# Optimization experiments

Measured on AMD Instinct MI355X. Metric: run time of the kernel, lower is better.

## Reference

```python
import jax, jax.numpy as jnp
import numpy as np

N_GRAPHS = 16
NPG = 420               # nodes per graph (fc1 expects 420*64 flatten)
N = N_GRAPHS * NPG      # 6720
DEG = 8
E = N * DEG             # 53760
HEADS = 4
IN_DIM = 2048
C1 = 1024               # per-head channels, layer 1
C2 = 64                 # layer 2 channels
OUT_DIM = 18
SLOPE = 0.2             # GATConv leaky_relu negative_slope


def _seg_softmax(scores, idx, n):
    # numerically-stable softmax over edges grouped by destination node
    m = jax.lax.stop_gradient(jax.ops.segment_max(scores, idx, num_segments=n))
    ex = jnp.exp(scores - m[idx])
    den = jax.ops.segment_sum(ex, idx, num_segments=n)
    return ex / (den[idx] + 1e-16)


def _transformer_conv(x, src, dst, wq, bq, wk, bk, wv, bv, ws, bs, heads, ch):
    # PyG TransformerConv defaults: concat=True, beta=False, root_weight=True, dropout=0
    n = x.shape[0]
    q = (x @ wq + bq).reshape(n, heads, ch)
    k = (x @ wk + bk).reshape(n, heads, ch)
    v = (x @ wv + bv).reshape(n, heads, ch)
    alpha = jnp.einsum('ehc,ehc->eh', q[dst], k[src]) / (ch ** 0.5)  # [E,H]
    alpha = _seg_softmax(alpha, dst, n)
    out = jax.ops.segment_sum(v[src] * alpha[..., None], dst, num_segments=n)  # [N,H,C]
    return out.reshape(n, heads * ch) + (x @ ws + bs)  # skip connection (lin_skip)


def _gat_conv(x, src, dst, w, a_src, a_dst, bias, heads, ch, concat):
    # PyG GATConv defaults: add_self_loops=True, negative_slope=0.2, lin has no bias
    n = x.shape[0]
    loop = jnp.arange(n, dtype=src.dtype)
    s = jnp.concatenate([src, loop])
    d = jnp.concatenate([dst, loop])
    h = (x @ w).reshape(n, heads, ch)
    es = jnp.einsum('nhc,hc->nh', h, a_src)
    ed = jnp.einsum('nhc,hc->nh', h, a_dst)
    e = jax.nn.leaky_relu(es[s] + ed[d], SLOPE)  # [E+N, H]
    alpha = _seg_softmax(e, d, n)
    out = jax.ops.segment_sum(h[s] * alpha[..., None], d, num_segments=n)  # [N,H,C]
    out = out.reshape(n, heads * ch) if concat else out.mean(axis=1)
    return out + bias


def setup_inputs() -> dict:
    key = jax.random.key(0)
    it = iter(jax.random.split(key, 64))
    def nrm(shape, scale):
        return jax.random.normal(next(it), shape, jnp.float32) * scale
    def lin(fi, fo):
        return nrm((fi, fo), float(1.0 / np.sqrt(fi)))
    p = {}
    p['x'] = nrm((N, IN_DIM), 1.0)
    p['edge_index'] = jax.random.randint(next(it), (2, E), 0, N, dtype=jnp.int32)
    for nm in ['t1_wq', 't1_wk', 't1_wv', 't1_ws']:
        p[nm] = lin(IN_DIM, HEADS * C1)
    for nm in ['t1_bq', 't1_bk', 't1_bv', 't1_bs']:
        p[nm] = jnp.zeros((HEADS * C1,), jnp.float32)
    # TransformerConv 2: 4096 -> 64, 1 head
    for nm in ['t2_wq', 't2_wk', 't2_wv', 't2_ws']:
        p[nm] = lin(HEADS * C1, C2)
    for nm in ['t2_bq', 't2_bk', 't2_bv', 't2_bs']:
        p[nm] = jnp.zeros((C2,), jnp.float32)
    p['g1_w'] = lin(IN_DIM, HEADS * C1)
    p['g1_as'] = nrm((HEADS, C1), 0.02)
    p['g1_ad'] = nrm((HEADS, C1), 0.02)
    p['g1_b'] = jnp.zeros((HEADS * C1,), jnp.float32)
    # GATConv 2: 4096 -> 64, 1 head, concat=False (mean)
    p['g2_w'] = lin(HEADS * C1, C2)
    p['g2_as'] = nrm((1, C2), 0.02)
    p['g2_ad'] = nrm((1, C2), 0.02)
    p['g2_b'] = jnp.zeros((C2,), jnp.float32)
    # MLP head
    p['fc1_w'] = lin(NPG * C2, 256); p['fc1_b'] = jnp.zeros((256,), jnp.float32)
    p['fc2_w'] = lin(256, 128);      p['fc2_b'] = jnp.zeros((128,), jnp.float32)
    p['fc3_w'] = lin(128, 64);       p['fc3_b'] = jnp.zeros((64,), jnp.float32)
    p['fc4_w'] = lin(64, OUT_DIM);   p['fc4_b'] = jnp.zeros((OUT_DIM,), jnp.float32)
    return p


def _forward(edge_index, x,
             t1_wq, t1_bq, t1_wk, t1_bk, t1_wv, t1_bv, t1_ws, t1_bs,
             t2_wq, t2_bq, t2_wk, t2_bk, t2_wv, t2_bv, t2_ws, t2_bs,
             g1_w, g1_as, g1_ad, g1_b, g2_w, g2_as, g2_ad, g2_b,
             fc1_w, fc1_b, fc2_w, fc2_b, fc3_w, fc3_b, fc4_w, fc4_b):
    src, dst = edge_index[0], edge_index[1]
    h = jax.nn.relu(_transformer_conv(x, src, dst, t1_wq, t1_bq, t1_wk, t1_bk,
                                      t1_wv, t1_bv, t1_ws, t1_bs, HEADS, C1))
    h = jax.nn.relu(_transformer_conv(h, src, dst, t2_wq, t2_bq, t2_wk, t2_bk,
                                      t2_wv, t2_bv, t2_ws, t2_bs, 1, C2))
    z = jax.nn.relu(_gat_conv(x, src, dst, g1_w, g1_as, g1_ad, g1_b, HEADS, C1, True))
    z = jax.nn.relu(_gat_conv(z, src, dst, g2_w, g2_as, g2_ad, g2_b, 1, C2, False))
    s = (h + z).reshape(-1, NPG * C2)          # [n_graphs, 26880]
    s = jax.nn.relu(s @ fc1_w + fc1_b)          # dropout = identity at eval
    s = jax.nn.relu(s @ fc2_w + fc2_b)
    s = jax.nn.relu(s @ fc3_w + fc3_b)
    return s @ fc4_w + fc4_b                    # [n_graphs, OUT_DIM]


def reference(x, edge_index,
              t1_wq, t1_bq, t1_wk, t1_bk, t1_wv, t1_bv, t1_ws, t1_bs,
              t2_wq, t2_bq, t2_wk, t2_bk, t2_wv, t2_bv, t2_ws, t2_bs,
              g1_w, g1_as, g1_ad, g1_b, g2_w, g2_as, g2_ad, g2_b,
              fc1_w, fc1_b, fc2_w, fc2_b, fc3_w, fc3_b, fc4_w, fc4_b):
    return _forward(edge_index, x,
                    t1_wq, t1_bq, t1_wk, t1_bk, t1_wv, t1_bv, t1_ws, t1_bs,
                    t2_wq, t2_bq, t2_wk, t2_bk, t2_wv, t2_bv, t2_ws, t2_bs,
                    g1_w, g1_as, g1_ad, g1_b, g2_w, g2_as, g2_ad, g2_b,
                    fc1_w, fc1_b, fc2_w, fc2_b, fc3_w, fc3_b, fc4_w, fc4_b)
```

## Files before the change

kernel.cpp:

```cpp
#include <hip/hip_runtime.h>
#include <stdint.h>
#include <stdio.h>

#define NNODES 6720
#define NEDGES 53760
#define NGRAPH 16
#define INDIM  2048
#define HEADS1 4
#define C1DIM  1024
#define D1     4096
#define C2DIM  64
#define N2     320
#define OUTDIM 18
#define SMCAP  256

typedef unsigned short u16;
typedef unsigned int   u32;

__device__ __forceinline__ float b2f(u16 u) {
  union { float f; u32 u; } v; v.u = ((u32)u) << 16; return v.f;
}
__device__ __forceinline__ u16 f2b(float f) {
  union { float f; u32 u; } v; v.f = f;
  u32 r = v.u + 0x7FFFu + ((v.u >> 16) & 1u);
  return (u16)(r >> 16);
}
__device__ __forceinline__ float ldf(const void* p, long i, int isf) {
  return isf ? ((const float*)p)[i] : b2f(((const u16*)p)[i]);
}

typedef __attribute__((ext_vector_type(8))) short bf16x8;
typedef __attribute__((ext_vector_type(4))) float f32x4;

__device__ __forceinline__ void gld_lds16(const u16* g, u16* l) {
  __builtin_amdgcn_global_load_lds((const __attribute__((address_space(1))) void*)g,
                                   (__attribute__((address_space(3))) void*)l, 16, 0, 0);
}

__global__ void detect_dtype(const u16* __restrict__ x, int* flag) {
  __shared__ int cnt;
  if (threadIdx.x == 0) cnt = 0;
  __syncthreads();
  int c = 0;
  for (int i = threadIdx.x; i < 4096; i += 256) {
    u16 u = x[2 * i];
    int e = (u >> 7) & 0xFF;
    if (e >= 118 && e <= 135) c++;
  }
  atomicAdd(&cnt, c);
  __syncthreads();
  if (threadIdx.x == 0) *flag = (cnt > 2048) ? 0 : 1;
}

__global__ void conv_any(const void* __restrict__ src, u16* __restrict__ dst,
                         long n, const int* __restrict__ flag) {
  long i = (long)blockIdx.x * 256 + threadIdx.x;
  long stride = (long)gridDim.x * 256;
  int isf = *flag;
  if (isf) {
    const float* s = (const float*)src;
    for (long j = i; j < n; j += stride) dst[j] = f2b(s[j]);
  } else {
    const u16* s = (const u16*)src;
    for (long j = i; j < n; j += stride) dst[j] = s[j];
  }
}

#define NSMALL 13
struct SmallConv {
  const void* src[NSMALL];
  u16*        dst[NSMALL];
  int         n[NSMALL];
};
__global__ void conv_small(SmallConv sc, const int* __restrict__ flag) {
  int b = blockIdx.x;
  int isf = *flag;
  const void* s = sc.src[b];
  u16* d = sc.dst[b];
  int n = sc.n[b];
  if (isf) {
    const float* sf = (const float*)s;
    for (int i = threadIdx.x; i < n; i += 256) d[i] = f2b(sf[i]);
  } else {
    const u16* sb = (const u16*)s;
    for (int i = threadIdx.x; i < n; i += 256) d[i] = sb[i];
  }
}

__global__ __launch_bounds__(256) void transpose_any(const void* __restrict__ src,
                                                     u16* __restrict__ dst,
                                                     int K, int Ncols,
                                                     const int* __restrict__ flag) {
  __shared__ u16 tile[32][33];
  int isf = *flag;
  int tx = threadIdx.x & 31, ty = threadIdx.x >> 5;
  int c0 = blockIdx.x * 32, r0 = blockIdx.y * 32;
  if (isf) {
    const float* s = (const float*)src;
    #pragma unroll
    for (int i = 0; i < 32; i += 8)
      tile[ty + i][tx] = f2b(s[(long)(r0 + ty + i) * Ncols + c0 + tx]);
  } else {
    const u16* s = (const u16*)src;
    #pragma unroll
    for (int i = 0; i < 32; i += 8)
      tile[ty + i][tx] = s[(long)(r0 + ty + i) * Ncols + c0 + tx];
  }
  __syncthreads();
  #pragma unroll
  for (int i = 0; i < 32; i += 8)
    dst[(long)(c0 + ty + i) * K + r0 + tx] = tile[tx][ty + i];
}

__global__ void pack_bias(const void* bq1, const void* bk1, const void* bv1, const void* bs1,
                          const void* bq2, const void* bk2, const void* bv2, const void* bs2,
                          float* bias1, float* bias2, const int* flag) {
  int isf = *flag;
  int i = blockIdx.x * 256 + threadIdx.x;
  if (i < 20480) {
    float v = 0.f;
    if (i < 4096) v = ldf(bq1, i, isf);
    else if (i < 8192)  v = ldf(bk1, i - 4096, isf);
    else if (i < 12288) v = ldf(bv1, i - 8192, isf);
    else if (i < 16384) v = ldf(bs1, i - 12288, isf);
    bias1[i] = v;
  } else if (i < 20480 + N2) {
    int j = i - 20480; float v = 0.f;
    if (j < 64) v = ldf(bq2, j, isf);
    else if (j < 128) v = ldf(bk2, j - 64, isf);
    else if (j < 192) v = ldf(bv2, j - 128, isf);
    else if (j < 256) v = ldf(bs2, j - 192, isf);
    bias2[j] = v;
  }
}

__global__ __launch_bounds__(256) void gemm_bt_r3(const u16* __restrict__ A,
                                                  const u16* __restrict__ BT,
                                                  const float* __restrict__ bias,
                                                  u16* __restrict__ C,
                                                  int M, int N, int K) {
  __shared__ u16 As[3][128 * 32];
  __shared__ u16 Bs[3][128 * 32];

  const int tid = threadIdx.x, lane = tid & 63, wave = tid >> 6;
  const int m0 = blockIdx.y * 128, n0 = blockIdx.x * 128;
  const int wm = (wave >> 1) * 64, wn = (wave & 1) * 64;

  const int srow = tid >> 2, scp = tid & 3;
  const int scl8 = (scp ^ ((srow >> 1) & 3)) * 8;
  int ar0 = m0 + srow;      if (ar0 >= M) ar0 = M - 1;
  int ar1 = m0 + srow + 64; if (ar1 >= M) ar1 = M - 1;
  const u16* ag0 = A + (long)ar0 * K + scl8;
  const u16* ag1 = A + (long)ar1 * K + scl8;
  const u16* bg0 = BT + (long)(n0 + srow) * K + scl8;
  const u16* bg1 = BT + (long)(n0 + srow + 64) * K + scl8;

  f32x4 acc[4][4];
  #pragma unroll
  for (int i = 0; i < 4; i++)
    #pragma unroll
    for (int j = 0; j < 4; j++) { f32x4 z = {0.f, 0.f, 0.f, 0.f}; acc[i][j] = z; }

  const int fr = lane & 15, q = lane >> 4;
  const int fq = (q ^ ((fr >> 1) & 3)) * 8;
  const int aoff = (wm + fr) * 32 + fq;
  const int boff = (wn + fr) * 32 + fq;

  const int NT = K >> 5;

  auto STAGE = [&](int t, int b) {
    const long k0 = (long)t * 32;
    gld_lds16(ag0 + k0, &As[b][(size_t)tid * 8]);
    gld_lds16(ag1 + k0, &As[b][2048 + (size_t)tid * 8]);
    gld_lds16(bg0 + k0, &Bs[b][(size_t)tid * 8]);
    gld_lds16(bg1 + k0, &Bs[b][2048 + (size_t)tid * 8]);
  };

  STAGE(0, 0); STAGE(1, 1);

  int cur = 0, nxt = 2;
  for (int t = 0; t < NT; ++t) {
    if (t < NT - 1) {
      asm volatile("s_waitcnt vmcnt(4)\n\ts_barrier" ::: "memory");
    } else {
      asm volatile("s_waitcnt vmcnt(0)\n\ts_barrier" ::: "memory");
    }
    if (t + 2 < NT) STAGE(t + 2, nxt);

    const u16* ab = &As[cur][0];
    const u16* bb = &Bs[cur][0];
    bf16x8 af[4], bfv[4];
    #pragma unroll
    for (int i = 0; i < 4; i++) af[i]  = *(const bf16x8*)(ab + aoff + i * 512);
    #pragma unroll
    for (int j = 0; j < 4; j++) bfv[j] = *(const bf16x8*)(bb + boff + j * 512);

    #pragma unroll
    for (int i = 0; i < 4; i++)
      #pragma unroll
      for (int j = 0; j < 4; j++)
        acc[i][j] = __builtin_amdgcn_mfma_f32_16x16x32_bf16(af[i], bfv[j], acc[i][j], 0, 0, 0);

    cur = (cur == 2) ? 0 : cur + 1;
    nxt = (nxt == 2) ? 0 : nxt + 1;
  }

  const int q4 = (lane >> 4) * 4, cl = lane & 15;
  #pragma unroll
  for (int i = 0; i < 4; i++)
    #pragma unroll
    for (int r = 0; r < 4; r++) {
      int row = m0 + wm + i * 16 + q4 + r;
      if (row < M) {
        #pragma unroll
        for (int j = 0; j < 4; j++) {
          int col = n0 + wn + j * 16 + cl;
          C[(long)row * N + col] = f2b(acc[i][j][r] + bias[col]);
        }
      }
    }
}

__global__ __launch_bounds__(256) void gemm2_64(const u16* __restrict__ h1,
                                                const u16* __restrict__ z1,
                                                const u16* __restrict__ wt2,
                                                const float* __restrict__ bias2,
                                                const u16* __restrict__ as64,
                                                const u16* __restrict__ ad64,
                                                u16* __restrict__ y2,
                                                float* __restrict__ es2,
                                                float* __restrict__ ed2) {
  __shared__ u16 As[64 * 64];
  __shared__ u16 Bs[64 * 64];
  const int nt = blockIdx.x;
  const u16* A = (nt < 4) ? h1 : z1;
  const u16* BT = wt2 + (size_t)nt * 64 * D1;
  const int m0 = blockIdx.y * 64, n0 = nt * 64;
  const int tid = threadIdx.x, lane = tid & 63, wave = tid >> 6;

  const int sr = tid >> 3, cp = tid & 7;
  const int cgl8 = (cp ^ (sr & 7)) * 8;
  const u16* ag0 = A + (long)(m0 + sr) * D1 + cgl8;
  const u16* ag1 = ag0 + (long)32 * D1;
  const u16* bg0 = BT + (long)sr * D1 + cgl8;
  const u16* bg1 = bg0 + (long)32 * D1;
  u16* al0 = As + tid * 8;  u16* al1 = As + 2048 + tid * 8;
  u16* bl0 = Bs + tid * 8;  u16* bl1 = Bs + 2048 + tid * 8;

  f32x4 acc[4];
  #pragma unroll
  for (int j = 0; j < 4; j++) { f32x4 z = {0.f, 0.f, 0.f, 0.f}; acc[j] = z; }

  const int fr = lane & 15, q = lane >> 4;
  const int x0 = ((q)     ^ (fr & 7)) * 8;
  const int x1 = ((4 + q) ^ (fr & 7)) * 8;
  const u16* apA = As + (wave * 16 + fr) * 64;

  for (int k0 = 0; k0 < D1; k0 += 64) {
    __syncthreads();
    gld_lds16(ag0 + k0, al0);
    gld_lds16(ag1 + k0, al1);
    gld_lds16(bg0 + k0, bl0);
    gld_lds16(bg1 + k0, bl1);
    __syncthreads();
    bf16x8 a0 = *(const bf16x8*)(apA + x0);
    bf16x8 a1 = *(const bf16x8*)(apA + x1);
    #pragma unroll
    for (int j = 0; j < 4; j++) {
      bf16x8 b0 = *(const bf16x8*)(Bs + (j * 16 + fr) * 64 + x0);
      acc[j] = __builtin_amdgcn_mfma_f32_16x16x32_bf16(a0, b0, acc[j], 0, 0, 0);
    }
    #pragma unroll
    for (int j = 0; j < 4; j++) {
      bf16x8 b1 = *(const bf16x8*)(Bs + (j * 16 + fr) * 64 + x1);
      acc[j] = __builtin_amdgcn_mfma_f32_16x16x32_bf16(a1, b1, acc[j], 0, 0, 0);
    }
  }
  const int q4 = (lane >> 4) * 4, cl = lane & 15;
  #pragma unroll
  for (int j = 0; j < 4; j++)
    #pragma unroll
    for (int r = 0; r < 4; r++) {
      int row = m0 + wave * 16 + q4 + r;
      int col = n0 + j * 16 + cl;
      y2[(long)row * N2 + col] = f2b(acc[j][r] + bias2[col]);
    }
  if (nt == 4) {
    #pragma unroll
    for (int r = 0; r < 4; r++) {
      int row = m0 + wave * 16 + q4 + r;
      float s1 = 0.f, s2 = 0.f;
      #pragma unroll
      for (int j = 0; j < 4; j++) {
        int col = j * 16 + cl;
        float v = b2f(f2b(acc[j][r] + bias2[256 + col]));
        s1 += v * b2f(as64[col]);
        s2 += v * b2f(ad64[col]);
      }
      #pragma unroll
      for (int o = 1; o < 16; o <<= 1) {
        s1 += __shfl_xor(s1, o, 64);
        s2 += __shfl_xor(s2, o, 64);
      }
      if (cl == 0) { es2[row] = s1; ed2[row] = s2; }
    }
  }
}

__global__ void zero_kernel(int* deg, float* f1sum) {
  int i = blockIdx.x * 256 + threadIdx.x;
  if (i < NNODES) deg[i] = 0;
  if (i < NGRAPH * 256) f1sum[i] = 0.f;
}

__global__ void count_deg(const int* __restrict__ ei, int* deg) {
  int e = blockIdx.x * 256 + threadIdx.x;
  if (e < NEDGES) atomicAdd(&deg[ei[NEDGES + e]], 1);
}

__global__ __launch_bounds__(1024) void scan_deg(const int* __restrict__ deg, int* off, int* cur) {
  __shared__ int sh[1024];
  const int t = threadIdx.x;
  const int PER = 7;
  int base = t * PER;
  int loc[PER];
  int sum = 0;
  #pragma unroll
  for (int i = 0; i < PER; i++) {
    int v = (base + i < NNODES) ? deg[base + i] : 0;
    loc[i] = sum; sum += v;
  }
  sh[t] = sum;
  __syncthreads();
  for (int d = 1; d < 1024; d <<= 1) {
    int v = (t >= d) ? sh[t - d] : 0;
    __syncthreads();
    sh[t] += v;
    __syncthreads();
  }
  int prev = (t > 0) ? sh[t - 1] : 0;
  #pragma unroll
  for (int i = 0; i < PER; i++) {
    int idx = base + i;
    if (idx <= NNODES) {
      int v = prev + loc[i];
      off[idx] = v;
      if (idx < NNODES) cur[idx] = v;
    }
  }
}

__global__ void scatter_edges(const int* __restrict__ ei, int* cur,
                              int* esrc, int* edst) {
  int e = blockIdx.x * 256 + threadIdx.x;
  if (e < NEDGES) {
    int s = ei[e], d = ei[NEDGES + e];
    int p = atomicAdd(&cur[d], 1);
    esrc[p] = s; edst[p] = d;
  }
}

__global__ __launch_bounds__(256) void t1_score_sm(const u16* __restrict__ yqk,
                                                   const int* __restrict__ off,
                                                   const int* __restrict__ esrc,
                                                   float* __restrict__ sc) {
  __shared__ float qsh[4096];
  __shared__ float sm[SMCAP * 4];
  int n = blockIdx.x, tid = threadIdx.x, lane = tid & 63, wave = tid >> 6;
  const u16* qr = yqk + (long)n * 8192;
  for (int i = tid * 8; i < 4096; i += 2048) {
    uint4 qa = *(const uint4*)(qr + i);
    const u16* qs = (const u16*)&qa;
    #pragma unroll
    for (int j = 0; j < 8; j++) qsh[i + j] = b2f(qs[j]);
  }
  __syncthreads();
  int p0 = off[n], p1 = off[n + 1], deg = p1 - p0;
  bool fits = (deg <= SMCAP);
  for (int p = p0 + wave; p < p1; p += 4) {
    const u16* k = yqk + (long)esrc[p] * 8192 + 4096;
    float dot[HEADS1];
    #pragma unroll
    for (int h = 0; h < HEADS1; h++) dot[h] = 0.f;
    #pragma unroll
    for (int h = 0; h < HEADS1; h++) {
      #pragma unroll
      for (int c = 0; c < 2; c++) {
        int idx = h * C1DIM + c * 512 + lane * 8;
        uint4 ka = *(const uint4*)(k + idx);
        const u16* ks = (const u16*)&ka;
        #pragma unroll
        for (int i = 0; i < 8; i++) dot[h] += qsh[idx + i] * b2f(ks[i]);
      }
    }
    #pragma unroll
    for (int h = 0; h < HEADS1; h++) {
      float v = dot[h];
      #pragma unroll
      for (int o = 32; o > 0; o >>= 1) v += __shfl_xor(v, o, 64);
      if (lane == 0) {
        float sv = v * (1.0f / 32.0f);
        if (fits) sm[(p - p0) * 4 + h] = sv;
        else      sc[(long)p * HEADS1 + h] = sv;
      }
    }
  }
  __syncthreads();
  if (fits) {
    int h = wave;
    float m = -3.4e38f;
    for (int e = lane; e < deg; e += 64) m = fmaxf(m, sm[e * 4 + h]);
    #pragma unroll
    for (int o = 32; o > 0; o >>= 1) m = fmaxf(m, __shfl_xor(m, o, 64));
    float s = 0.f;
    for (int e = lane; e < deg; e += 64) {
      float ex = __expf(sm[e * 4 + h] - m);
      sm[e * 4 + h] = ex; s += ex;
    }
    #pragma unroll
    for (int o = 32; o > 0; o >>= 1) s += __shfl_xor(s, o, 64);
    float inv = 1.0f / (s + 1e-16f);
    for (int e = lane; e < deg; e += 64)
      sc[(long)(p0 + e) * 4 + h] = sm[e * 4 + h] * inv;
  } else if (tid < 4) {
    int h = tid;
    float m = -3.4e38f;
    for (int p = p0; p < p1; p++) m = fmaxf(m, sc[(long)p * 4 + h]);
    float s = 0.f;
    for (int p = p0; p < p1; p++) {
      float ex = __expf(sc[(long)p * 4 + h] - m);
      sc[(long)p * 4 + h] = ex; s += ex;
    }
    float inv = 1.0f / (s + 1e-16f);
    for (int p = p0; p < p1; p++) sc[(long)p * 4 + h] *= inv;
  }
}

__global__ __launch_bounds__(256) void t1_agg(const u16* __restrict__ yvs,
                                              const int* __restrict__ off,
                                              const int* __restrict__ esrc,
                                              const float* __restrict__ alpha,
                                              u16* __restrict__ h1) {
  int n = blockIdx.x, t = threadIdx.x, h = t >> 6;
  int p0 = off[n], p1 = off[n + 1];
  float acc[16];
  #pragma unroll
  for (int i = 0; i < 16; i++) acc[i] = 0.f;
  for (int p = p0; p < p1; p++) {
    float a = alpha[p * 4 + h];
    const u16* v = yvs + (long)esrc[p] * 8192 + t * 16;
    uint4 v0 = *(const uint4*)(v);
    uint4 v1 = *(const uint4*)(v + 8);
    const u16* s0 = (const u16*)&v0; const u16* s1 = (const u16*)&v1;
    #pragma unroll
    for (int i = 0; i < 8; i++) acc[i] += a * b2f(s0[i]);
    #pragma unroll
    for (int i = 0; i < 8; i++) acc[8 + i] += a * b2f(s1[i]);
  }
  const u16* sk = yvs + (long)n * 8192 + 4096 + t * 16;
  uint4 k0 = *(const uint4*)(sk); uint4 k1 = *(const uint4*)(sk + 8);
  const u16* ks0 = (const u16*)&k0; const u16* ks1 = (const u16*)&k1;
  u16 outv[16];
  #pragma unroll
  for (int i = 0; i < 8; i++) outv[i] = f2b(fmaxf(acc[i] + b2f(ks0[i]), 0.f));
  #pragma unroll
  for (int i = 0; i < 8; i++) outv[8 + i] = f2b(fmaxf(acc[8 + i] + b2f(ks1[i]), 0.f));
  *(uint4*)(h1 + (long)n * D1 + t * 16) = *(uint4*)outv;
  *(uint4*)(h1 + (long)n * D1 + t * 16 + 8) = *(uint4*)(outv + 8);
}

__global__ __launch_bounds__(256) void g1_dots(const u16* __restrict__ gat,
                                               const u16* __restrict__ a_src,
                                               const u16* __restrict__ a_dst,
                                               float* __restrict__ es, float* __restrict__ ed) {
  int n = blockIdx.x;
  int h = threadIdx.x >> 6, lane = threadIdx.x & 63;
  const u16* hr = gat + (long)n * D1 + h * C1DIM;
  const u16* as = a_src + h * C1DIM;
  const u16* ad = a_dst + h * C1DIM;
  float s1 = 0.f, s2 = 0.f;
  #pragma unroll
  for (int c = 0; c < 2; c++) {
    int idx = c * 512 + lane * 8;
    uint4 hv = *(const uint4*)(hr + idx);
    uint4 av = *(const uint4*)(as + idx);
    uint4 dv = *(const uint4*)(ad + idx);
    const u16* hs = (const u16*)&hv; const u16* a1 = (const u16*)&av; const u16* d1 = (const u16*)&dv;
    #pragma unroll
    for (int i = 0; i < 8; i++) {
      float x = b2f(hs[i]);
      s1 += x * b2f(a1[i]); s2 += x * b2f(d1[i]);
    }
  }
  #pragma unroll
  for (int o = 32; o > 0; o >>= 1) { s1 += __shfl_xor(s1, o, 64); s2 += __shfl_xor(s2, o, 64); }
  if (lane == 0) { es[n * 4 + h] = s1; ed[n * 4 + h] = s2; }
}

__global__ __launch_bounds__(256) void g1_score_sm(const int* __restrict__ off,
                                                   const int* __restrict__ esrc,
                                                   const float* __restrict__ es,
                                                   const float* __restrict__ ed,
                                                   float* __restrict__ sc,
                                                   float* __restrict__ selfsc) {
  __shared__ float sm[SMCAP * 4];
  int n = blockIdx.x, tid = threadIdx.x, lane = tid & 63, wave = tid >> 6;
  int p0 = off[n], p1 = off[n + 1], deg = p1 - p0;
  bool fits = (deg <= SMCAP);
  for (int idx = tid; idx < deg * 4; idx += 256) {
    int e = idx >> 2, h = idx & 3;
    float v = es[esrc[p0 + e] * 4 + h] + ed[n * 4 + h];
    v = (v > 0.f) ? v : 0.2f * v;
    if (fits) sm[idx] = v;
    else      sc[(long)(p0 + e) * 4 + h] = v;
  }
  __syncthreads();
  if (fits) {
    int h = wave;
    float sv = es[n * 4 + h] + ed[n * 4 + h];
    sv = (sv > 0.f) ? sv : 0.2f * sv;
    float m = sv;
    for (int e = lane; e < deg; e += 64) m = fmaxf(m, sm[e * 4 + h]);
    #pragma unroll
    for (int o = 32; o > 0; o >>= 1) m = fmaxf(m, __shfl_xor(m, o, 64));
    float s = 0.f;
    for (int e = lane; e < deg; e += 64) {
      float ex = __expf(sm[e * 4 + h] - m);
      sm[e * 4 + h] = ex; s += ex;
    }
    #pragma unroll
    for (int o = 32; o > 0; o >>= 1) s += __shfl_xor(s, o, 64);
    float selfe = __expf(sv - m);
    float inv = 1.0f / (s + selfe + 1e-16f);
    for (int e = lane; e < deg; e += 64)
      sc[(long)(p0 + e) * 4 + h] = sm[e * 4 + h] * inv;
    if (lane == 0) selfsc[n * 4 + h] = selfe * inv;
  } else if (tid < 4) {
    int h = tid;
    float sv = es[n * 4 + h] + ed[n * 4 + h];
    sv = (sv > 0.f) ? sv : 0.2f * sv;
    float m = sv;
    for (int p = p0; p < p1; p++) m = fmaxf(m, sc[(long)p * 4 + h]);
    float s = 0.f;
    for (int p = p0; p < p1; p++) {
      float ex = __expf(sc[(long)p * 4 + h] - m);
      sc[(long)p * 4 + h] = ex; s += ex;
    }
    float selfe = __expf(sv - m);
    float inv = 1.0f / (s + selfe + 1e-16f);
    for (int p = p0; p < p1; p++) sc[(long)p * 4 + h] *= inv;
    selfsc[n * 4 + h] = selfe * inv;
  }
}

__global__ __launch_bounds__(256) void g1_agg(const u16* __restrict__ gat,
                                              const int* __restrict__ off,
                                              const int* __restrict__ esrc,
                                              const float* __restrict__ alpha,
                                              const float* __restrict__ selfa,
                                              const u16* __restrict__ bias,
                                              u16* __restrict__ z1) {
  int n = blockIdx.x, t = threadIdx.x, h = t >> 6;
  int p0 = off[n], p1 = off[n + 1];
  float acc[16];
  #pragma unroll
  for (int i = 0; i < 16; i++) acc[i] = 0.f;
  for (int p = p0; p < p1; p++) {
    float a = alpha[p * 4 + h];
    const u16* v = gat + (long)esrc[p] * D1 + t * 16;
    uint4 v0 = *(const uint4*)(v);
    uint4 v1 = *(const uint4*)(v + 8);
    const u16* s0 = (const u16*)&v0; const u16* s1 = (const u16*)&v1;
    #pragma unroll
    for (int i = 0; i < 8; i++) acc[i] += a * b2f(s0[i]);
    #pragma unroll
    for (int i = 0; i < 8; i++) acc[8 + i] += a * b2f(s1[i]);
  }
  {
    float a = selfa[n * 4 + h];
    const u16* v = gat + (long)n * D1 + t * 16;
    uint4 v0 = *(const uint4*)(v);
    uint4 v1 = *(const uint4*)(v + 8);
    const u16* s0 = (const u16*)&v0; const u16* s1 = (const u16*)&v1;
    #pragma unroll
    for (int i = 0; i < 8; i++) acc[i] += a * b2f(s0[i]);
    #pragma unroll
    for (int i = 0; i < 8; i++) acc[8 + i] += a * b2f(s1[i]);
  }
  u16 outv[16];
  #pragma unroll
  for (int i = 0; i < 16; i++) outv[i] = f2b(fmaxf(acc[i] + b2f(bias[t * 16 + i]), 0.f));
  *(uint4*)(z1 + (long)n * D1 + t * 16) = *(uint4*)outv;
  *(uint4*)(z1 + (long)n * D1 + t * 16 + 8) = *(uint4*)(outv + 8);
}

__global__ __launch_bounds__(256) void t2g2_score_sm(const u16* __restrict__ y2,
                                                     const int* __restrict__ off,
                                                     const int* __restrict__ esrc,
                                                     const float* __restrict__ es2,
                                                     const float* __restrict__ ed2,
                                                     float* __restrict__ scT,
                                                     float* __restrict__ scG,
                                                     float* __restrict__ sfG) {
  __shared__ float smT[SMCAP];
  __shared__ float smG[SMCAP];
  int n = blockIdx.x, tid = threadIdx.x, lane = tid & 63, wave = tid >> 6;
  int p0 = off[n], p1 = off[n + 1], deg = p1 - p0;
  bool fits = (deg <= SMCAP);
  float qv = b2f(y2[(long)n * N2 + lane]);
  float edn = ed2[n];
  for (int e = wave; e < deg; e += 4) {
    int s = esrc[p0 + e];
    float kv = b2f(y2[(long)s * N2 + C2DIM + lane]);
    float d = qv * kv;
    #pragma unroll
    for (int o = 32; o > 0; o >>= 1) d += __shfl_xor(d, o, 64);
    if (lane == 0) {
      float vt = d * 0.125f;
      float vg = es2[s] + edn;
      vg = (vg > 0.f) ? vg : 0.2f * vg;
      if (fits) { smT[e] = vt; smG[e] = vg; }
      else      { scT[p0 + e] = vt; scG[p0 + e] = vg; }
    }
  }
  __syncthreads();
  if (fits) {
    if (wave == 0) {
      float m = -3.4e38f;
      for (int e = lane; e < deg; e += 64) m = fmaxf(m, smT[e]);
      #pragma unroll
      for (int o = 32; o > 0; o >>= 1) m = fmaxf(m, __shfl_xor(m, o, 64));
      float s = 0.f;
      for (int e = lane; e < deg; e += 64) { float ex = __expf(smT[e] - m); smT[e] = ex; s += ex; }
      #pragma unroll
      for (int o = 32; o > 0; o >>= 1) s += __shfl_xor(s, o, 64);
      float inv = 1.0f / (s + 1e-16f);
      for (int e = lane; e < deg; e += 64) scT[p0 + e] = smT[e] * inv;
    } else if (wave == 1) {
      float sv = es2[n] + edn;
      sv = (sv > 0.f) ? sv : 0.2f * sv;
      float m = sv;
      for (int e = lane; e < deg; e += 64) m = fmaxf(m, smG[e]);
      #pragma unroll
      for (int o = 32; o > 0; o >>= 1) m = fmaxf(m, __shfl_xor(m, o, 64));
      float s = 0.f;
      for (int e = lane; e < deg; e += 64) { float ex = __expf(smG[e] - m); smG[e] = ex; s += ex; }
      #pragma unroll
      for (int o = 32; o > 0; o >>= 1) s += __shfl_xor(s, o, 64);
      float selfe = __expf(sv - m);
      float inv = 1.0f / (s + selfe + 1e-16f);
      for (int e = lane; e < deg; e += 64) scG[p0 + e] = smG[e] * inv;
      if (lane == 0) sfG[n] = selfe * inv;
    }
  } else {
    if (tid == 0) {
      float m = -3.4e38f;
      for (int p = p0; p < p1; p++) m = fmaxf(m, scT[p]);
      float s = 0.f;
      for (int p = p0; p < p1; p++) { float ex = __expf(scT[p] - m); scT[p] = ex; s += ex; }
      float inv = 1.0f / (s + 1e-16f);
      for (int p = p0; p < p1; p++) scT[p] *= inv;
    } else if (tid == 1) {
      float sv = es2[n] + edn;
      sv = (sv > 0.f) ? sv : 0.2f * sv;
      float m = sv;
      for (int p = p0; p < p1; p++) m = fmaxf(m, scG[p]);
      float s = 0.f;
      for (int p = p0; p < p1; p++) { float ex = __expf(scG[p] - m); scG[p] = ex; s += ex; }
      float selfe = __expf(sv - m);
      float inv = 1.0f / (s + selfe + 1e-16f);
      for (int p = p0; p < p1; p++) scG[p] *= inv;
      sfG[n] = selfe * inv;
    }
  }
}

__global__ __launch_bounds__(256) void tg2_agg(const u16* __restrict__ y2,
                                               const int* __restrict__ off,
                                               const int* __restrict__ esrc,
                                               const float* __restrict__ alphaT,
                                               const float* __restrict__ alphaG,
                                               const float* __restrict__ selfaG,
                                               const u16* __restrict__ bias,
                                               float* __restrict__ sn) {
  int n = (blockIdx.x * 256 + threadIdx.x) >> 6, lane = threadIdx.x & 63;
  if (n >= NNODES) return;
  int p0 = off[n], p1 = off[n + 1];
  float at = 0.f, ag = 0.f;
  for (int p = p0; p < p1; p++) {
    const u16* row = y2 + (long)esrc[p] * N2;
    at += alphaT[p] * b2f(row[2 * C2DIM + lane]);
    ag += alphaG[p] * b2f(row[4 * C2DIM + lane]);
  }
  at += b2f(y2[(long)n * N2 + 3 * C2DIM + lane]);
  ag += selfaG[n] * b2f(y2[(long)n * N2 + 4 * C2DIM + lane]);
  sn[(long)n * C2DIM + lane] = fmaxf(at, 0.f) + fmaxf(ag + b2f(bias[lane]), 0.f);
}

#define FCHUNK 210
__global__ __launch_bounds__(256) void fc1_partial(const float* __restrict__ sn,
                                                   const void* __restrict__ w,
                                                   const int* __restrict__ flag,
                                                   float* __restrict__ f1sum) {
  __shared__ float sl[16 * FCHUNK];
  int k0 = blockIdx.x * FCHUNK;
  int t = threadIdx.x;
  int isf = *flag;
  for (int idx = t; idx < 16 * FCHUNK; idx += 256) {
    int g = idx / FCHUNK, kk = idx - g * FCHUNK;
    sl[idx] = sn[(long)g * 26880 + k0 + kk];
  }
  __syncthreads();
  float acc[16];
  #pragma unroll
  for (int g = 0; g < 16; g++) acc[g] = 0.f;
  if (isf) {
    const float* wf = (const float*)w;
    for (int kk = 0; kk < FCHUNK; kk++) {
      float wv = wf[(long)(k0 + kk) * 256 + t];
      #pragma unroll
      for (int g = 0; g < 16; g++) acc[g] += sl[g * FCHUNK + kk] * wv;
    }
  } else {
    const u16* wb = (const u16*)w;
    for (int kk = 0; kk < FCHUNK; kk++) {
      float wv = b2f(wb[(long)(k0 + kk) * 256 + t]);
      #pragma unroll
      for (int g = 0; g < 16; g++) acc[g] += sl[g * FCHUNK + kk] * wv;
    }
  }
  #pragma unroll
  for (int g = 0; g < 16; g++) atomicAdd(&f1sum[g * 256 + t], acc[g]);
}

__global__ __launch_bounds__(256) void fc_tail(const float* __restrict__ f1sum,
                                               const u16* b1, const u16* w2, const u16* b2,
                                               const u16* w3, const u16* b3,
                                               const u16* w4, const u16* b4,
                                               void* __restrict__ out,
                                               const int* __restrict__ flag) {
  __shared__ float A1[16 * 256];
  __shared__ float A2[16 * 128];
  __shared__ float A3[16 * 64];
  int isf = *flag;
  int t = threadIdx.x;
  for (int i = t; i < 4096; i += 256) A1[i] = fmaxf(f1sum[i] + b2f(b1[i & 255]), 0.f);
  __syncthreads();
  for (int i = t; i < 2048; i += 256) {
    int g = i >> 7, j = i & 127;
    float acc = b2f(b2[j]);
    for (int k = 0; k < 256; k++) acc += A1[g * 256 + k] * b2f(w2[k * 128 + j]);
    A2[i] = fmaxf(acc, 0.f);
  }
  __syncthreads();
  for (int i = t; i < 1024; i += 256) {
    int g = i >> 6, j = i & 63;
    float acc = b2f(b3[j]);
    for (int k = 0; k < 128; k++) acc += A2[g * 128 + k] * b2f(w3[k * 64 + j]);
    A3[i] = fmaxf(acc, 0.f);
  }
  __syncthreads();
  for (int i = t; i < NGRAPH * OUTDIM; i += 256) {
    int g = i / OUTDIM, j = i - g * OUTDIM;
    float acc = b2f(b4[j]);
    for (int k = 0; k < 64; k++) acc += A3[g * 64 + k] * b2f(w4[k * OUTDIM + j]);
    if (isf) ((float*)out)[i] = acc;
    else     ((u16*)out)[i] = f2b(acc);
  }
}

extern "C" void kernel_launch(void* const* d_in, const int* in_sizes, int n_in,
                              void* d_out, int out_size, void* d_ws, size_t ws_size,
                              hipStream_t stream) {
  const void* x     = d_in[0];
  const int*  ei    = (const int*)d_in[1];
  const void* t1_wq = d_in[2];
  const void* t1_wk = d_in[3];
  const void* t1_wv = d_in[4];
  const void* t1_ws = d_in[5];
  const void* t1_bq = d_in[6];
  const void* t1_bk = d_in[7];
  const void* t1_bv = d_in[8];
  const void* t1_bs = d_in[9];
  const void* t2_wq = d_in[10];
  const void* t2_wk = d_in[11];
  const void* t2_wv = d_in[12];
  const void* t2_ws = d_in[13];
  const void* t2_bq = d_in[14];
  const void* t2_bk = d_in[15];
  const void* t2_bv = d_in[16];
  const void* t2_bs = d_in[17];
  const void* g1_w  = d_in[18];
  const void* g1_as = d_in[19];
  const void* g1_ad = d_in[20];
  const void* g1_b  = d_in[21];
  const void* g2_w  = d_in[22];
  const void* g2_as = d_in[23];
  const void* g2_ad = d_in[24];
  const void* g2_b  = d_in[25];
  const void* fc1_w = d_in[26];
  const void* fc1_b = d_in[27];
  const void* fc2_w = d_in[28];
  const void* fc2_b = d_in[29];
  const void* fc3_w = d_in[30];
  const void* fc3_b = d_in[31];
  const void* fc4_w = d_in[32];
  const void* fc4_b = d_in[33];

  char* wp = (char*)d_ws;
  auto alloc = [&](size_t bytes) {
    char* p = wp; wp += (bytes + 255) & ~(size_t)255; return p;
  };
  u16*   wtSlab = (u16*)  alloc((size_t)8192 * INDIM * 2);
  u16*   wt2    = (u16*)  alloc((size_t)N2 * D1 * 2);
  u16*   yqk    = (u16*)  alloc((size_t)NNODES * 8192 * 2);
  u16*   h1     = (u16*)  alloc((size_t)NNODES * D1 * 2);
  u16*   y2     = (u16*)  alloc((size_t)NNODES * N2 * 2);
  u16*   xb     = (u16*)  alloc((size_t)NNODES * INDIM * 2);
  u16*   fc2wb  = (u16*)  alloc((size_t)256 * 128 * 2);
  u16*   fc3wb  = (u16*)  alloc((size_t)128 * 64 * 2);
  u16*   fc4wb  = (u16*)  alloc((size_t)64 * OUTDIM * 2);
  u16*   fb1    = (u16*)  alloc(256 * 2);
  u16*   fb2    = (u16*)  alloc(128 * 2);
  u16*   fb3    = (u16*)  alloc(64 * 2);
  u16*   fb4    = (u16*)  alloc(OUTDIM * 2);
  u16*   g1asb  = (u16*)  alloc(4096 * 2);
  u16*   g1adb  = (u16*)  alloc(4096 * 2);
  u16*   g1bb   = (u16*)  alloc(4096 * 2);
  u16*   g2asb  = (u16*)  alloc(64 * 2);
  u16*   g2adb  = (u16*)  alloc(64 * 2);
  u16*   g2bb   = (u16*)  alloc(64 * 2);
  float* bias1  = (float*)alloc((size_t)20480 * 4);
  float* bias2  = (float*)alloc((size_t)N2 * 4);
  int*   flag   = (int*)  alloc(256);
  int*   deg    = (int*)  alloc((size_t)NNODES * 4);
  int*   off    = (int*)  alloc((size_t)(NNODES + 1) * 4);
  int*   cur    = (int*)  alloc((size_t)NNODES * 4);
  int*   esrc   = (int*)  alloc((size_t)NEDGES * 4);
  int*   edst   = (int*)  alloc((size_t)NEDGES * 4);
  float* scT1   = (float*)alloc((size_t)NEDGES * 4 * 4);
  float* esG1   = (float*)alloc((size_t)NNODES * 4 * 4);
  float* edG1   = (float*)alloc((size_t)NNODES * 4 * 4);
  float* scG1   = (float*)alloc((size_t)NEDGES * 4 * 4);
  float* sfG1   = (float*)alloc((size_t)NNODES * 4 * 4);
  float* scT2   = (float*)alloc((size_t)NEDGES * 4);
  float* scG2   = (float*)alloc((size_t)NEDGES * 4);
  float* sfG2   = (float*)alloc((size_t)NNODES * 4);
  float* es2    = (float*)alloc((size_t)NNODES * 4);
  float* ed2    = (float*)alloc((size_t)NNODES * 4);
  float* sn     = (float*)alloc((size_t)NNODES * C2DIM * 4);
  float* f1sum  = (float*)alloc((size_t)NGRAPH * 256 * 4);

  u16* gat = yqk;
  u16* z1  = yqk + (size_t)NNODES * D1;

  size_t need = (size_t)(wp - (char*)d_ws);
  if (ws_size < need) {
    fprintf(stderr, "[GATGT kernel] WORKSPACE TOO SMALL ws=%zu need=%zu\n", ws_size, need);
    return;
  }

  detect_dtype<<<1, 256, 0, stream>>>((const u16*)x, flag);

  zero_kernel<<<27, 256, 0, stream>>>(deg, f1sum);
  count_deg<<<NEDGES / 256, 256, 0, stream>>>(ei, deg);
  scan_deg<<<1, 1024, 0, stream>>>(deg, off, cur);
  scatter_edges<<<NEDGES / 256, 256, 0, stream>>>(ei, cur, esrc, edst);
  pack_bias<<<82, 256, 0, stream>>>(t1_bq, t1_bk, t1_bv, t1_bs,
                                    t2_bq, t2_bk, t2_bv, t2_bs, bias1, bias2, flag);

  conv_any<<<4096, 256, 0, stream>>>(x, xb, (long)NNODES * INDIM, flag);
  {
    SmallConv sc;
    const void* srcs[NSMALL] = { fc2_w, fc3_w, fc4_w, fc1_b, fc2_b, fc3_b, fc4_b,
                                 g1_as, g1_ad, g1_b, g2_as, g2_ad, g2_b };
    u16* dsts[NSMALL] = { fc2wb, fc3wb, fc4wb, fb1, fb2, fb3, fb4,
                          g1asb, g1adb, g1bb, g2asb, g2adb, g2bb };
    int  ns[NSMALL]   = { 256 * 128, 128 * 64, 64 * OUTDIM, 256, 128, 64, OUTDIM,
                          4096, 4096, 4096, 64, 64, 64 };
    for (int i = 0; i < NSMALL; i++) { sc.src[i] = srcs[i]; sc.dst[i] = dsts[i]; sc.n[i] = ns[i]; }
    conv_small<<<NSMALL, 256, 0, stream>>>(sc, flag);
  }

  transpose_any<<<dim3(128, 64), 256, 0, stream>>>(t1_wq, wtSlab, INDIM, 4096, flag);
  transpose_any<<<dim3(128, 64), 256, 0, stream>>>(t1_wk, wtSlab + (size_t)4096 * INDIM, INDIM, 4096, flag);
  gemm_bt_r3<<<dim3(64, 53), 256, 0, stream>>>(xb, wtSlab, bias1, yqk, NNODES, 8192, INDIM);
  t1_score_sm<<<NNODES, 256, 0, stream>>>(yqk, off, esrc, scT1);

  transpose_any<<<dim3(128, 64), 256, 0, stream>>>(t1_wv, wtSlab, INDIM, 4096, flag);
  transpose_any<<<dim3(128, 64), 256, 0, stream>>>(t1_ws, wtSlab + (size_t)4096 * INDIM, INDIM, 4096, flag);
  gemm_bt_r3<<<dim3(64, 53), 256, 0, stream>>>(xb, wtSlab, bias1 + 8192, yqk, NNODES, 8192, INDIM);
  t1_agg<<<NNODES, 256, 0, stream>>>(yqk, off, esrc, scT1, h1);

  transpose_any<<<dim3(128, 64), 256, 0, stream>>>(g1_w, wtSlab, INDIM, 4096, flag);
  gemm_bt_r3<<<dim3(32, 53), 256, 0, stream>>>(xb, wtSlab, bias1 + 16384, gat, NNODES, 4096, INDIM);
  g1_dots<<<NNODES, 256, 0, stream>>>(gat, g1asb, g1adb, esG1, edG1);
  g1_score_sm<<<NNODES, 256, 0, stream>>>(off, esrc, esG1, edG1, scG1, sfG1);
  g1_agg<<<NNODES, 256, 0, stream>>>(gat, off, esrc, scG1, sfG1, g1bb, z1);

  {
    const void* srcs2[5] = { t2_wq, t2_wk, t2_wv, t2_ws, g2_w };
    for (int s = 0; s < 5; s++)
      transpose_any<<<dim3(2, 128), 256, 0, stream>>>(
          srcs2[s], wt2 + (size_t)s * 64 * D1, D1, 64, flag);
  }
  gemm2_64<<<dim3(5, NNODES / 64), 256, 0, stream>>>(h1, z1, wt2, bias2,
                                                     g2asb, g2adb, y2, es2, ed2);

  t2g2_score_sm<<<NNODES, 256, 0, stream>>>(y2, off, esrc, es2, ed2, scT2, scG2, sfG2);
  tg2_agg<<<NNODES / 4, 256, 0, stream>>>(y2, off, esrc, scT2, scG2, sfG2, g2bb, sn);

  fc1_partial<<<128, 256, 0, stream>>>(sn, fc1_w, flag, f1sum);
  fc_tail<<<1, 256, 0, stream>>>(f1sum, fb1, fc2wb, fb2, fc3wb, fb3,
                                 fc4wb, fb4, d_out, flag);
}
```

Baseline: 1.473 ms.

## Fuse GAT attention dots into GEMM epilogue, batch transposes, pipeline gemm2

After: 1.543 ms. 4.8% more time.

```diff
diff --git a/kernel.cpp b/kernel.cpp
--- a/kernel.cpp
+++ b/kernel.cpp
@@ -87,11 +87,13 @@
   }
 }
 
-__global__ __launch_bounds__(256) void transpose_any(const void* __restrict__ src,
-                                                     u16* __restrict__ dst,
-                                                     int K, int Ncols,
-                                                     const int* __restrict__ flag) {
+#define NTP 5
+struct TPB { const void* src[NTP]; u16* dst[NTP]; };
+__global__ __launch_bounds__(256) void transpose_batch(TPB tb, int K, int Ncols,
+                                                       const int* __restrict__ flag) {
   __shared__ u16 tile[32][33];
+  const void* src = tb.src[blockIdx.z];
+  u16* dst = tb.dst[blockIdx.z];
   int isf = *flag;
   int tx = threadIdx.x & 31, ty = threadIdx.x >> 5;
   int c0 = blockIdx.x * 32, r0 = blockIdx.y * 32;
@@ -138,7 +140,11 @@
                                                   const u16* __restrict__ BT,
                                                   const float* __restrict__ bias,
                                                   u16* __restrict__ C,
-                                                  int M, int N, int K) {
+                                                  int M, int N, int K,
+                                                  const u16* __restrict__ as4096,
+                                                  const u16* __restrict__ ad4096,
+                                                  float* __restrict__ esOut,
+                                                  float* __restrict__ edOut) {
   __shared__ u16 As[3][128 * 32];
   __shared__ u16 Bs[3][128 * 32];
 
@@ -219,6 +225,34 @@
         }
       }
     }
+  if (esOut) {
+    const int h = (n0 + wn) >> 10;
+    #pragma unroll
+    for (int i = 0; i < 4; i++)
+      #pragma unroll
+      for (int r = 0; r < 4; r++) {
+        int row = m0 + wm + i * 16 + q4 + r;
+        if (row < M) {
+          float s1 = 0.f, s2 = 0.f;
+          #pragma unroll
+          for (int j = 0; j < 4; j++) {
+            int col = n0 + wn + j * 16 + cl;
+            float v = b2f(f2b(acc[i][j][r] + bias[col]));
+            s1 += v * b2f(as4096[col]);
+            s2 += v * b2f(ad4096[col]);
+          }
+          #pragma unroll
+          for (int o = 1; o < 16; o <<= 1) {
+            s1 += __shfl_xor(s1, o, 64);
+            s2 += __shfl_xor(s2, o, 64);
+          }
+          if (cl == 0) {
+            atomicAdd(&esOut[row * 4 + h], s1);
+            atomicAdd(&edOut[row * 4 + h], s2);
+          }
+        }
+      }
+  }
 }
 
 __global__ __launch_bounds__(256) void gemm2_64(const u16* __restrict__ h1,
@@ -230,8 +264,8 @@
                                                 u16* __restrict__ y2,
                                                 float* __restrict__ es2,
                                                 float* __restrict__ ed2) {
-  __shared__ u16 As[64 * 64];
-  __shared__ u16 Bs[64 * 64];
+  __shared__ u16 As[3][64 * 64];
+  __shared__ u16 Bs[3][64 * 64];
   const int nt = blockIdx.x;
   const u16* A = (nt < 4) ? h1 : z1;
   const u16* BT = wt2 + (size_t)nt * 64 * D1;
@@ -244,8 +278,6 @@
   const u16* ag1 = ag0 + (long)32 * D1;
   const u16* bg0 = BT + (long)sr * D1 + cgl8;
   const u16* bg1 = bg0 + (long)32 * D1;
-  u16* al0 = As + tid * 8;  u16* al1 = As + 2048 + tid * 8;
-  u16* bl0 = Bs + tid * 8;  u16* bl1 = Bs + 2048 + tid * 8;
 
   f32x4 acc[4];
   #pragma unroll
@@ -254,28 +286,48 @@
   const int fr = lane & 15, q = lane >> 4;
   const int x0 = ((q)     ^ (fr & 7)) * 8;
   const int x1 = ((4 + q) ^ (fr & 7)) * 8;
-  const u16* apA = As + (wave * 16 + fr) * 64;
-
-  for (int k0 = 0; k0 < D1; k0 += 64) {
-    __syncthreads();
-    gld_lds16(ag0 + k0, al0);
-    gld_lds16(ag1 + k0, al1);
-    gld_lds16(bg0 + k0, bl0);
-    gld_lds16(bg1 + k0, bl1);
-    __syncthreads();
-    bf16x8 a0 = *(const bf16x8*)(apA + x0);
-    bf16x8 a1 = *(const bf16x8*)(apA + x1);
+  const int apA = (wave * 16 + fr) * 64;
+
+  const int NT = D1 >> 6;
+
+  auto STAGE = [&](int t, int b) {
+    const long k0 = (long)t * 64;
+    gld_lds16(ag0 + k0, &As[b][(size_t)tid * 8]);
+    gld_lds16(ag1 + k0, &As[b][2048 + (size_t)tid * 8]);
+    gld_lds16(bg0 + k0, &Bs[b][(size_t)tid * 8]);
+    gld_lds16(bg1 + k0, &Bs[b][2048 + (size_t)tid * 8]);
+  };
+
+  STAGE(0, 0); STAGE(1, 1);
+
+  int cur = 0, nxt = 2;
+  for (int t = 0; t < NT; ++t) {
+    if (t < NT - 1) {
+      asm volatile("s_waitcnt vmcnt(4)\n\ts_barrier" ::: "memory");
+    } else {
+      asm volatile("s_waitcnt vmcnt(0)\n\ts_barrier" ::: "memory");
+    }
+    if (t + 2 < NT) STAGE(t + 2, nxt);
+
+    const u16* ab = &As[cur][0];
+    const u16* bb = &Bs[cur][0];
+    bf16x8 a0 = *(const bf16x8*)(ab + apA + x0);
+    bf16x8 a1 = *(const bf16x8*)(ab + apA + x1);
     #pragma unroll
     for (int j = 0; j < 4; j++) {
-      bf16x8 b0 = *(const bf16x8*)(Bs + (j * 16 + fr) * 64 + x0);
+      bf16x8 b0 = *(const bf16x8*)(bb + (j * 16 + fr) * 64 + x0);
       acc[j] = __builtin_amdgcn_mfma_f32_16x16x32_bf16(a0, b0, acc[j], 0, 0, 0);
     }
     #pragma unroll
     for (int j = 0; j < 4; j++) {
-      bf16x8 b1 = *(const bf16x8*)(Bs + (j * 16 + fr) * 64 + x1);
+      bf16x8 b1 = *(const bf16x8*)(bb + (j * 16 + fr) * 64 + x1);
       acc[j] = __builtin_amdgcn_mfma_f32_16x16x32_bf16(a1, b1, acc[j], 0, 0, 0);
     }
-  }
+
+    cur = (cur == 2) ? 0 : cur + 1;
+    nxt = (nxt == 2) ? 0 : nxt + 1;
+  }
+
   const int q4 = (lane >> 4) * 4, cl = lane & 15;
   #pragma unroll
   for (int j = 0; j < 4; j++)
@@ -307,10 +359,11 @@
   }
 }
 
-__global__ void zero_kernel(int* deg, float* f1sum) {
+__global__ void zero_kernel(int* deg, float* f1sum, float* esG1, float* edG1) {
   int i = blockIdx.x * 256 + threadIdx.x;
   if (i < NNODES) deg[i] = 0;
   if (i < NGRAPH * 256) f1sum[i] = 0.f;
+  if (i < NNODES * 4) { esG1[i] = 0.f; edG1[i] = 0.f; }
 }
 
 __global__ void count_deg(const int* __restrict__ ei, int* deg) {
@@ -467,34 +520,6 @@
   for (int i = 0; i < 8; i++) outv[8 + i] = f2b(fmaxf(acc[8 + i] + b2f(ks1[i]), 0.f));
   *(uint4*)(h1 + (long)n * D1 + t * 16) = *(uint4*)outv;
   *(uint4*)(h1 + (long)n * D1 + t * 16 + 8) = *(uint4*)(outv + 8);
-}
-
-__global__ __launch_bounds__(256) void g1_dots(const u16* __restrict__ gat,
-                                               const u16* __restrict__ a_src,
-                                               const u16* __restrict__ a_dst,
-                                               float* __restrict__ es, float* __restrict__ ed) {
-  int n = blockIdx.x;
-  int h = threadIdx.x >> 6, lane = threadIdx.x & 63;
-  const u16* hr = gat + (long)n * D1 + h * C1DIM;
-  const u16* as = a_src + h * C1DIM;
-  const u16* ad = a_dst + h * C1DIM;
-  float s1 = 0.f, s2 = 0.f;
-  #pragma unroll
-  for (int c = 0; c < 2; c++) {
-    int idx = c * 512 + lane * 8;
-    uint4 hv = *(const uint4*)(hr + idx);
-    uint4 av = *(const uint4*)(as + idx);
-    uint4 dv = *(const uint4*)(ad + idx);
-    const u16* hs = (const u16*)&hv; const u16* a1 = (const u16*)&av; const u16* d1 = (const u16*)&dv;
-    #pragma unroll
-    for (int i = 0; i < 8; i++) {
-      float x = b2f(hs[i]);
-      s1 += x * b2f(a1[i]); s2 += x * b2f(d1[i]);
-    }
-  }
-  #pragma unroll
-  for (int o = 32; o > 0; o >>= 1) { s1 += __shfl_xor(s1, o, 64); s2 += __shfl_xor(s2, o, 64); }
-  if (lane == 0) { es[n * 4 + h] = s1; ed[n * 4 + h] = s2; }
 }
 
 __global__ __launch_bounds__(256) void g1_score_sm(const int* __restrict__ off,
@@ -862,7 +887,7 @@
 
   detect_dtype<<<1, 256, 0, stream>>>((const u16*)x, flag);
 
-  zero_kernel<<<27, 256, 0, stream>>>(deg, f1sum);
+  zero_kernel<<<105, 256, 0, stream>>>(deg, f1sum, esG1, edG1);
   count_deg<<<NEDGES / 256, 256, 0, stream>>>(ei, deg);
   scan_deg<<<1, 1024, 0, stream>>>(deg, off, cur);
   scatter_edges<<<NEDGES / 256, 256, 0, stream>>>(ei, cur, esrc, edst);
@@ -882,27 +907,41 @@
     conv_small<<<NSMALL, 256, 0, stream>>>(sc, flag);
   }
 
-  transpose_any<<<dim3(128, 64), 256, 0, stream>>>(t1_wq, wtSlab, INDIM, 4096, flag);
-  transpose_any<<<dim3(128, 64), 256, 0, stream>>>(t1_wk, wtSlab + (size_t)4096 * INDIM, INDIM, 4096, flag);
-  gemm_bt_r3<<<dim3(64, 53), 256, 0, stream>>>(xb, wtSlab, bias1, yqk, NNODES, 8192, INDIM);
+  {
+    TPB tb{};
+    tb.src[0] = t1_wq; tb.dst[0] = wtSlab;
+    tb.src[1] = t1_wk; tb.dst[1] = wtSlab + (size_t)4096 * INDIM;
+    transpose_batch<<<dim3(128, 64, 2), 256, 0, stream>>>(tb, INDIM, 4096, flag);
+  }
+  gemm_bt_r3<<<dim3(64, 53), 256, 0, stream>>>(xb, wtSlab, bias1, yqk, NNODES, 8192, INDIM,
+                                               nullptr, nullptr, nullptr, nullptr);
   t1_score_sm<<<NNODES, 256, 0, stream>>>(yqk, off, esrc, scT1);
 
-  transpose_any<<<dim3(128, 64), 256, 0, stream>>>(t1_wv, wtSlab, INDIM, 4096, flag);
-  transpose_any<<<dim3(128, 64), 256, 0, stream>>>(t1_ws, wtSlab + (size_t)4096 * INDIM, INDIM, 4096, flag);
-  gemm_bt_r3<<<dim3(64, 53), 256, 0, stream>>>(xb, wtSlab, bias1 + 8192, yqk, NNODES, 8192, INDIM);
+  {
+    TPB tb{};
+    tb.src[0] = t1_wv; tb.dst[0] = wtSlab;
+    tb.src[1] = t1_ws; tb.dst[1] = wtSlab + (size_t)4096 * INDIM;
+    transpose_batch<<<dim3(128, 64, 2), 256, 0, stream>>>(tb, INDIM, 4096, flag);
+  }
+  gemm_bt_r3<<<dim3(64, 53), 256, 0, stream>>>(xb, wtSlab, bias1 + 8192, yqk, NNODES, 8192, INDIM,
+                                               nullptr, nullptr, nullptr, nullptr);
   t1_agg<<<NNODES, 256, 0, stream>>>(yqk, off, esrc, scT1, h1);
 
-  transpose_any<<<dim3(128, 64), 256, 0, stream>>>(g1_w, wtSlab, INDIM, 4096, flag);
-  gemm_bt_r3<<<dim3(32, 53), 256, 0, stream>>>(xb, wtSlab, bias1 + 16384, gat, NNODES, 4096, INDIM);
-  g1_dots<<<NNODES, 256, 0, stream>>>(gat, g1asb, g1adb, esG1, edG1);
+  {
+    TPB tb{};
+    tb.src[0] = g1_w; tb.dst[0] = wtSlab;
+    transpose_batch<<<dim3(128, 64, 1), 256, 0, stream>>>(tb, INDIM, 4096, flag);
+  }
+  gemm_bt_r3<<<dim3(32, 53), 256, 0, stream>>>(xb, wtSlab, bias1 + 16384, gat, NNODES, 4096, INDIM,
+                                               g1asb, g1adb, esG1, edG1);
   g1_score_sm<<<NNODES, 256, 0, stream>>>(off, esrc, esG1, edG1, scG1, sfG1);
   g1_agg<<<NNODES, 256, 0, stream>>>(gat, off, esrc, scG1, sfG1, g1bb, z1);
 
   {
+    TPB tb{};
     const void* srcs2[5] = { t2_wq, t2_wk, t2_wv, t2_ws, g2_w };
-    for (int s = 0; s < 5; s++)
-      transpose_any<<<dim3(2, 128), 256, 0, stream>>>(
-          srcs2[s], wt2 + (size_t)s * 64 * D1, D1, 64, flag);
+    for (int s = 0; s < 5; s++) { tb.src[s] = srcs2[s]; tb.dst[s] = wt2 + (size_t)s * 64 * D1; }
+    transpose_batch<<<dim3(2, 128, 5), 256, 0, stream>>>(tb, D1, 64, flag);
   }
   gemm2_64<<<dim3(5, NNODES / 64), 256, 0, stream>>>(h1, z1, wt2, bias2,
                                                      g2asb, g2adb, y2, es2, ed2);
```
